# Kernel optimization log

Measured on AMD Instinct MI355X. Metric: run time of the kernel, lower is better.

## Reference

```python
import jax, jax.numpy as jnp
import numpy as np

NEG_INF = -1e9


def setup_inputs() -> dict:
    key = jax.random.key(0)
    k1, k2, k3 = jax.random.split(key, 3)
    B, S, D, N, K = 8, 4096, 1024, 128, 8
    hidden_states = jax.random.normal(k1, (B, S, D), dtype=jnp.float32)
    sentence_indicator = jnp.sort(
        jax.random.randint(k2, (B, S), 0, N), axis=-1).astype(jnp.int64)
    cls_w = jax.random.normal(k3, (D,), dtype=jnp.float32) * (1.0 / np.sqrt(D))
    cls_b = jnp.zeros((), dtype=jnp.float32)
    return {
        "hidden_states": hidden_states,
        "sentence_indicator": sentence_indicator,
        "cls_w": cls_w,
        "cls_b": cls_b,
        "num_sentences": N,
        "extraction_k": K,
    }


def _selection_loop(hidden_states, sentence_indicator, cls_w, cls_b,
                    num_sentences, extraction_k):
    # --- sentence segment-sum pooling (replaces per-sentence masked-sum loop) ---
    seg_sum = jax.vmap(
        lambda h, ind: jax.ops.segment_sum(h, ind, num_segments=num_sentences)
    )(hidden_states, sentence_indicator)               # [B, N, D]
    counts = jax.vmap(
        lambda ind: jax.ops.segment_sum(
            jnp.ones(ind.shape, jnp.float32), ind, num_segments=num_sentences)
    )(sentence_indicator)                              # [B, N]
    sentence_lens = jnp.clip(counts, 1.0)[..., None]   # [B, N, 1], clamp(min=1)
    sentence_mask0 = (counts > 0).astype(jnp.float32)  # valid-sentence mask [B, N]

    B, N, D = seg_sum.shape

    def step(carry, _):
        cur_sum, cur_len, smask, sel = carry
        combined = cur_sum[:, None, :] + seg_sum           # [B, N, D]
        combined_len = cur_len[:, None, :] + sentence_lens  # [B, N, 1]
        pooled = combined / combined_len                    # [B, N, D]
        logits = jnp.einsum('bnd,d->bn', pooled, cls_w) + cls_b
        logits = jnp.where(smask > 0, logits, NEG_INF)      # mask_tensor
        idx = jnp.argmax(logits, axis=-1)                   # eval path (argmax)
        one_hot = jax.nn.one_hot(idx, N, dtype=jnp.float32)  # [B, N]
        smask = (1.0 - one_hot) * smask
        new_sum = jnp.einsum('bn,bnd->bd', one_hot, combined)
        new_len = jnp.sum(one_hot[..., None] * combined_len, axis=1)  # [B, 1]
        return (new_sum, new_len, smask, sel + one_hot), logits

    init = (jnp.zeros((B, D), jnp.float32),
            jnp.zeros((B, 1), jnp.float32),
            sentence_mask0,
            jnp.zeros((B, N), jnp.float32))
    (_, _, _, selected), all_logits = jax.lax.scan(
        step, init, None, length=extraction_k)
    selected = jnp.clip(selected, 0.0, 1.0)  # clamp(max=1)
    return selected, all_logits  # [B,N], [K,B,N]


def reference(hidden_states, sentence_indicator, cls_w, cls_b,
              num_sentences, extraction_k):
    selected_one_hot, all_logits = _selection_loop(
        hidden_states, sentence_indicator, cls_w, cls_b,
        num_sentences, extraction_k)
    # convert_attention_mask: token is kept iff its sentence was selected
    new_attention_mask = jnp.take_along_axis(
        selected_one_hot, sentence_indicator, axis=1)      # [B, S] float 0/1
    masked_hidden_states = new_attention_mask[..., None] * hidden_states
    return selected_one_hot, all_logits, new_attention_mask, masked_hidden_states
```

## Files before the change

### kernel.cpp

```cpp
#include <hip/hip_runtime.h>

#define B_ 8
#define S_ 4096
#define D_ 1024
#define N_ 128
#define K_ 8
#define NEG_INF_ (-1e9f)

__global__ void tok_dot_kernel(const float* __restrict__ h,
                               const float* __restrict__ cls_w,
                               float* __restrict__ tok_dot) {
    const int lane = threadIdx.x & 63;
    const int gw = (blockIdx.x << 2) + (threadIdx.x >> 6);
    const int dofs = lane * 4;

    const float4 w0 = *reinterpret_cast<const float4*>(cls_w + 0 * 256 + dofs);
    const float4 w1 = *reinterpret_cast<const float4*>(cls_w + 1 * 256 + dofs);
    const float4 w2 = *reinterpret_cast<const float4*>(cls_w + 2 * 256 + dofs);
    const float4 w3 = *reinterpret_cast<const float4*>(cls_w + 3 * 256 + dofs);

    for (int token = gw; token < B_ * S_; token += 8192) {
        const float* p = h + (size_t)token * D_;
        const float4 v0 = *reinterpret_cast<const float4*>(p + 0 * 256 + dofs);
        const float4 v1 = *reinterpret_cast<const float4*>(p + 1 * 256 + dofs);
        const float4 v2 = *reinterpret_cast<const float4*>(p + 2 * 256 + dofs);
        const float4 v3 = *reinterpret_cast<const float4*>(p + 3 * 256 + dofs);
        float acc = v0.x * w0.x + v0.y * w0.y + v0.z * w0.z + v0.w * w0.w
                  + v1.x * w1.x + v1.y * w1.y + v1.z * w1.z + v1.w * w1.w
                  + v2.x * w2.x + v2.y * w2.y + v2.z * w2.z + v2.w * w2.w
                  + v3.x * w3.x + v3.y * w3.y + v3.z * w3.z + v3.w * w3.w;
        for (int off = 32; off > 0; off >>= 1) acc += __shfl_down(acc, off, 64);
        if (lane == 0) tok_dot[token] = acc;
    }
}

__global__ void select_kernel(const float* __restrict__ tok_dot,
                              const int* __restrict__ ind,
                              const float* __restrict__ cls_b,
                              float* __restrict__ out_selected,
                              float* __restrict__ out_logits,
                              float* __restrict__ sel_ws) {
    const int b = blockIdx.x;
    const int tid = threadIdx.x;

    __shared__ float td[S_];
    __shared__ int   si[S_];
    __shared__ float red_val[N_];
    __shared__ int   red_idx[N_];
    __shared__ float s_dotcur, s_lencur;

    for (int s = tid; s < S_; s += 256) {
        td[s] = tok_dot[b * S_ + s];
        si[s] = ind[b * S_ + s];
    }
    if (tid == 0) { s_dotcur = 0.f; s_lencur = 0.f; }
    __syncthreads();

    float dseg = 0.f, len = 1.f, smask = 0.f, sel = 0.f;
    if (tid < N_) {
        const int n = tid;
        int lo = 0, hi = S_;
        while (lo < hi) { int mid = (lo + hi) >> 1; if (si[mid] < n) lo = mid + 1; else hi = mid; }
        const int s0 = lo;
        lo = s0; hi = S_;
        while (lo < hi) { int mid = (lo + hi) >> 1; if (si[mid] < n + 1) lo = mid + 1; else hi = mid; }
        const int s1 = lo;
        float acc = 0.f;
        for (int s = s0; s < s1; ++s) acc += td[s];
        dseg  = acc;
        len   = fmaxf((float)(s1 - s0), 1.0f);
        smask = (s1 > s0) ? 1.f : 0.f;
    }
    const float bias = cls_b[0];
    __syncthreads();

    for (int k = 0; k < K_; ++k) {
        if (tid < N_) {
            float logit = (s_dotcur + dseg) / (s_lencur + len) + bias;
            logit = (smask > 0.f) ? logit : NEG_INF_;
            out_logits[(size_t)k * (B_ * N_) + b * N_ + tid] = logit;
            red_val[tid] = logit;
            red_idx[tid] = tid;
        }
        __syncthreads();
        for (int off = 64; off > 0; off >>= 1) {
            if (tid < off) {
                float v2 = red_val[tid + off]; int i2 = red_idx[tid + off];
                if (v2 > red_val[tid] || (v2 == red_val[tid] && i2 < red_idx[tid])) {
                    red_val[tid] = v2; red_idx[tid] = i2;
                }
            }
            __syncthreads();
        }
        const int pick = red_idx[0];
        if (tid == pick) {
            smask = 0.f; sel = 1.f;
            s_dotcur += dseg;
            s_lencur += len;
        }
        __syncthreads();
    }

    if (tid < N_) {
        out_selected[b * N_ + tid] = sel;
        sel_ws[b * N_ + tid] = sel;
    }
}

__global__ void mask_kernel(const float* __restrict__ h,
                            const int* __restrict__ ind,
                            const float* __restrict__ sel_ws,
                            float* __restrict__ out_mask,
                            float* __restrict__ out_masked) {
    const int t0 = blockIdx.x << 2;
    const int tid = threadIdx.x;
    #pragma unroll
    for (int i = 0; i < 4; ++i) {
        const int token = t0 + i;
        const int b = token >> 12;
        const float m = sel_ws[b * N_ + ind[token]];
        if (tid == 0) out_mask[token] = m;
        const size_t base = (size_t)token * D_ + tid * 4;
        if (m == 0.f) {
            *reinterpret_cast<float4*>(out_masked + base) = make_float4(0.f, 0.f, 0.f, 0.f);
        } else {
            const float4 v = *reinterpret_cast<const float4*>(h + base);
            *reinterpret_cast<float4*>(out_masked + base) =
                make_float4(v.x * m, v.y * m, v.z * m, v.w * m);
        }
    }
}

extern "C" void kernel_launch(void* const* d_in, const int* in_sizes, int n_in,
                              void* d_out, int out_size, void* d_ws, size_t ws_size,
                              hipStream_t stream) {
    const float* h     = (const float*)d_in[0];
    const int*   ind   = (const int*)d_in[1];
    const float* cls_w = (const float*)d_in[2];
    const float* cls_b = (const float*)d_in[3];

    float* out = (float*)d_out;
    float* out_selected = out;
    float* out_logits   = out + 1024;
    float* out_mask     = out + 1024 + 8192;
    float* out_masked   = out + 1024 + 8192 + 32768;

    char* ws = (char*)d_ws;
    float* tok_dot = (float*)ws;
    float* sel_ws  = (float*)(ws + (size_t)B_ * S_ * 4);

    tok_dot_kernel<<<dim3(2048), dim3(256), 0, stream>>>(h, cls_w, tok_dot);
    select_kernel<<<dim3(B_), dim3(256), 0, stream>>>(tok_dot, ind, cls_b,
                                                      out_selected, out_logits, sel_ws);
    mask_kernel<<<dim3(B_ * S_ / 4), dim3(256), 0, stream>>>(h, ind, sel_ws, out_mask, out_masked);
}
```

Baseline: 58.44 us.

## Zero-fill masked output separately and copy only selected sentence rows

The per-token mask kernel is replaced by three steps: a bulk zero-fill of the masked output, the selection kernel now also writing the token mask and the token ranges of the picked sentences, and a sparse copy kernel that copies only the selected tokens' hidden rows. Since only K of N sentences are selected, most rows need no read of the hidden states. This avoids the per-token indicator lookup and the full hidden-state read for unselected tokens. The cost is an extra full-size write pass plus another launch, and every sparse-copy block recomputes prefix counts from the ranges.

```diff
diff --git a/kernel.cpp b/kernel.cpp
--- a/kernel.cpp
+++ b/kernel.cpp
@@ -6,6 +6,13 @@
 #define N_ 128
 #define K_ 8
 #define NEG_INF_ (-1e9f)
+
+__global__ void zero_fill_kernel(float4* __restrict__ p, int n4) {
+    int i = blockIdx.x * blockDim.x + threadIdx.x;
+    const int stride = gridDim.x * blockDim.x;
+    const float4 z = make_float4(0.f, 0.f, 0.f, 0.f);
+    for (; i < n4; i += stride) p[i] = z;
+}
 
 __global__ void tok_dot_kernel(const float* __restrict__ h,
                                const float* __restrict__ cls_w,
@@ -39,7 +46,8 @@
                               const float* __restrict__ cls_b,
                               float* __restrict__ out_selected,
                               float* __restrict__ out_logits,
-                              float* __restrict__ sel_ws) {
+                              float* __restrict__ out_mask,
+                              int* __restrict__ ranges) {
     const int b = blockIdx.x;
     const int tid = threadIdx.x;
 
@@ -48,6 +56,9 @@
     __shared__ float red_val[N_];
     __shared__ int   red_idx[N_];
     __shared__ float s_dotcur, s_lencur;
+    __shared__ int   s_picks[K_];
+    __shared__ int   seg0[N_], seg1[N_];
+    __shared__ float sel_sh[N_];
 
     for (int s = tid; s < S_; s += 256) {
         td[s] = tok_dot[b * S_ + s];
@@ -65,6 +76,7 @@
         lo = s0; hi = S_;
         while (lo < hi) { int mid = (lo + hi) >> 1; if (si[mid] < n + 1) lo = mid + 1; else hi = mid; }
         const int s1 = lo;
+        seg0[tid] = s0; seg1[tid] = s1;
         float acc = 0.f;
         for (int s = s0; s < s1; ++s) acc += td[s];
         dseg  = acc;
@@ -97,37 +109,58 @@
             smask = 0.f; sel = 1.f;
             s_dotcur += dseg;
             s_lencur += len;
+            s_picks[k] = pick;
         }
         __syncthreads();
     }
 
     if (tid < N_) {
+        sel_sh[tid] = sel;
         out_selected[b * N_ + tid] = sel;
-        sel_ws[b * N_ + tid] = sel;
+    }
+    __syncthreads();
+    if (tid < K_) {
+        const int p = s_picks[tid];
+        ranges[(b * K_ + tid) * 2]     = seg0[p];
+        ranges[(b * K_ + tid) * 2 + 1] = seg1[p];
+    }
+    for (int s = tid; s < S_; s += 256) {
+        out_mask[b * S_ + s] = sel_sh[si[s]];
     }
 }
 
-__global__ void mask_kernel(const float* __restrict__ h,
-                            const int* __restrict__ ind,
-                            const float* __restrict__ sel_ws,
-                            float* __restrict__ out_mask,
-                            float* __restrict__ out_masked) {
-    const int t0 = blockIdx.x << 2;
+__global__ void sparse_copy_kernel(const float* __restrict__ h,
+                                   const int* __restrict__ ranges,
+                                   float* __restrict__ out_masked) {
+    int bpref[B_ + 1];
+    bpref[0] = 0;
+    #pragma unroll
+    for (int b = 0; b < B_; ++b) {
+        int c = 0;
+        #pragma unroll
+        for (int k = 0; k < K_; ++k)
+            c += ranges[(b * K_ + k) * 2 + 1] - ranges[(b * K_ + k) * 2];
+        bpref[b + 1] = bpref[b] + c;
+    }
+    const int total = bpref[B_];
     const int tid = threadIdx.x;
-    #pragma unroll
-    for (int i = 0; i < 4; ++i) {
-        const int token = t0 + i;
-        const int b = token >> 12;
-        const float m = sel_ws[b * N_ + ind[token]];
-        if (tid == 0) out_mask[token] = m;
-        const size_t base = (size_t)token * D_ + tid * 4;
-        if (m == 0.f) {
-            *reinterpret_cast<float4*>(out_masked + base) = make_float4(0.f, 0.f, 0.f, 0.f);
-        } else {
-            const float4 v = *reinterpret_cast<const float4*>(h + base);
-            *reinterpret_cast<float4*>(out_masked + base) =
-                make_float4(v.x * m, v.y * m, v.z * m, v.w * m);
+
+    for (int w = blockIdx.x; w < total; w += gridDim.x) {
+        int b = 0;
+        while (w >= bpref[b + 1]) ++b;
+        int off = w - bpref[b];
+        int s = 0;
+        #pragma unroll
+        for (int k = 0; k < K_; ++k) {
+            const int s0 = ranges[(b * K_ + k) * 2];
+            const int s1 = ranges[(b * K_ + k) * 2 + 1];
+            const int l = s1 - s0;
+            if (off < l) { s = s0 + off; off = 0x7fffffff; }
+            else if (off != 0x7fffffff) off -= l;
         }
+        const size_t base = ((size_t)b * S_ + s) * D_ + tid * 4;
+        *reinterpret_cast<float4*>(out_masked + base) =
+            *reinterpret_cast<const float4*>(h + base);
     }
 }
 
@@ -147,10 +180,14 @@
 
     char* ws = (char*)d_ws;
     float* tok_dot = (float*)ws;
-    float* sel_ws  = (float*)(ws + (size_t)B_ * S_ * 4);
+    int*   ranges  = (int*)(ws + (size_t)B_ * S_ * 4);
 
+    const int n4 = B_ * S_ * D_ / 4;
+    zero_fill_kernel<<<dim3(2048), dim3(256), 0, stream>>>(
+        reinterpret_cast<float4*>(out_masked), n4);
     tok_dot_kernel<<<dim3(2048), dim3(256), 0, stream>>>(h, cls_w, tok_dot);
     select_kernel<<<dim3(B_), dim3(256), 0, stream>>>(tok_dot, ind, cls_b,
-                                                      out_selected, out_logits, sel_ws);
-    mask_kernel<<<dim3(B_ * S_ / 4), dim3(256), 0, stream>>>(h, ind, sel_ws, out_mask, out_masked);
+                                                      out_selected, out_logits,
+                                                      out_mask, ranges);
+    sparse_copy_kernel<<<dim3(2048), dim3(256), 0, stream>>>(h, ranges, out_masked);
 }
```

After: 63.89 us. +9.3%, slower.

## Warp-level argmax in selection, move mask gather into select kernel, batch tokens

Applied to the files above, without the earlier changes.

The selection loop now runs in a single 64-lane wavefront, with each lane owning two sentences and doing the argmax through shuffles, so the shared-memory tree reduction and its many block barriers are gone. The select kernel also writes the per-token attention mask directly, which lets the final write kernel read one precomputed mask value per token instead of gathering indicator and selection per token. It also processes 8 tokens per block and copies h without multiplying, which is valid because the mask is 0 or 1. The tok_dot kernel unrolls two independent tokens per iteration to raise memory-level parallelism. The cost is extra serial work in the 8-block select kernel, which now also writes the mask.

```diff
diff --git a/kernel.cpp b/kernel.cpp
--- a/kernel.cpp
+++ b/kernel.cpp
@@ -19,18 +19,33 @@
     const float4 w2 = *reinterpret_cast<const float4*>(cls_w + 2 * 256 + dofs);
     const float4 w3 = *reinterpret_cast<const float4*>(cls_w + 3 * 256 + dofs);
 
-    for (int token = gw; token < B_ * S_; token += 8192) {
-        const float* p = h + (size_t)token * D_;
-        const float4 v0 = *reinterpret_cast<const float4*>(p + 0 * 256 + dofs);
-        const float4 v1 = *reinterpret_cast<const float4*>(p + 1 * 256 + dofs);
-        const float4 v2 = *reinterpret_cast<const float4*>(p + 2 * 256 + dofs);
-        const float4 v3 = *reinterpret_cast<const float4*>(p + 3 * 256 + dofs);
-        float acc = v0.x * w0.x + v0.y * w0.y + v0.z * w0.z + v0.w * w0.w
-                  + v1.x * w1.x + v1.y * w1.y + v1.z * w1.z + v1.w * w1.w
-                  + v2.x * w2.x + v2.y * w2.y + v2.z * w2.z + v2.w * w2.w
-                  + v3.x * w3.x + v3.y * w3.y + v3.z * w3.z + v3.w * w3.w;
-        for (int off = 32; off > 0; off >>= 1) acc += __shfl_down(acc, off, 64);
-        if (lane == 0) tok_dot[token] = acc;
+    #pragma unroll
+    for (int t = 0; t < 2; ++t) {
+        const int tokA = gw + t * 16384;
+        const int tokB = tokA + 8192;
+        const float* pA = h + (size_t)tokA * D_;
+        const float* pB = h + (size_t)tokB * D_;
+        const float4 a0 = *reinterpret_cast<const float4*>(pA + 0 * 256 + dofs);
+        const float4 a1 = *reinterpret_cast<const float4*>(pA + 1 * 256 + dofs);
+        const float4 a2 = *reinterpret_cast<const float4*>(pA + 2 * 256 + dofs);
+        const float4 a3 = *reinterpret_cast<const float4*>(pA + 3 * 256 + dofs);
+        const float4 b0 = *reinterpret_cast<const float4*>(pB + 0 * 256 + dofs);
+        const float4 b1 = *reinterpret_cast<const float4*>(pB + 1 * 256 + dofs);
+        const float4 b2 = *reinterpret_cast<const float4*>(pB + 2 * 256 + dofs);
+        const float4 b3 = *reinterpret_cast<const float4*>(pB + 3 * 256 + dofs);
+        float accA = a0.x * w0.x + a0.y * w0.y + a0.z * w0.z + a0.w * w0.w
+                   + a1.x * w1.x + a1.y * w1.y + a1.z * w1.z + a1.w * w1.w
+                   + a2.x * w2.x + a2.y * w2.y + a2.z * w2.z + a2.w * w2.w
+                   + a3.x * w3.x + a3.y * w3.y + a3.z * w3.z + a3.w * w3.w;
+        float accB = b0.x * w0.x + b0.y * w0.y + b0.z * w0.z + b0.w * w0.w
+                   + b1.x * w1.x + b1.y * w1.y + b1.z * w1.z + b1.w * w1.w
+                   + b2.x * w2.x + b2.y * w2.y + b2.z * w2.z + b2.w * w2.w
+                   + b3.x * w3.x + b3.y * w3.y + b3.z * w3.z + b3.w * w3.w;
+        for (int off = 32; off > 0; off >>= 1) {
+            accA += __shfl_down(accA, off, 64);
+            accB += __shfl_down(accB, off, 64);
+        }
+        if (lane == 0) { tok_dot[tokA] = accA; tok_dot[tokB] = accB; }
     }
 }
 
@@ -39,24 +54,20 @@
                               const float* __restrict__ cls_b,
                               float* __restrict__ out_selected,
                               float* __restrict__ out_logits,
-                              float* __restrict__ sel_ws) {
+                              float* __restrict__ out_mask) {
     const int b = blockIdx.x;
     const int tid = threadIdx.x;
 
     __shared__ float td[S_];
     __shared__ int   si[S_];
-    __shared__ float red_val[N_];
-    __shared__ int   red_idx[N_];
-    __shared__ float s_dotcur, s_lencur;
+    __shared__ float sh_dseg[N_], sh_len[N_], sh_msk[N_], sh_sel[N_];
 
     for (int s = tid; s < S_; s += 256) {
         td[s] = tok_dot[b * S_ + s];
         si[s] = ind[b * S_ + s];
     }
-    if (tid == 0) { s_dotcur = 0.f; s_lencur = 0.f; }
     __syncthreads();
 
-    float dseg = 0.f, len = 1.f, smask = 0.f, sel = 0.f;
     if (tid < N_) {
         const int n = tid;
         int lo = 0, hi = S_;
@@ -67,66 +78,70 @@
         const int s1 = lo;
         float acc = 0.f;
         for (int s = s0; s < s1; ++s) acc += td[s];
-        dseg  = acc;
-        len   = fmaxf((float)(s1 - s0), 1.0f);
-        smask = (s1 > s0) ? 1.f : 0.f;
+        sh_dseg[tid] = acc;
+        sh_len[tid]  = fmaxf((float)(s1 - s0), 1.0f);
+        sh_msk[tid]  = (s1 > s0) ? 1.f : 0.f;
     }
-    const float bias = cls_b[0];
     __syncthreads();
 
-    for (int k = 0; k < K_; ++k) {
-        if (tid < N_) {
-            float logit = (s_dotcur + dseg) / (s_lencur + len) + bias;
-            logit = (smask > 0.f) ? logit : NEG_INF_;
-            out_logits[(size_t)k * (B_ * N_) + b * N_ + tid] = logit;
-            red_val[tid] = logit;
-            red_idx[tid] = tid;
+    if (tid < 64) {
+        const float bias = cls_b[0];
+        const float d0 = sh_dseg[tid],      d1 = sh_dseg[tid + 64];
+        const float l0 = sh_len[tid],       l1 = sh_len[tid + 64];
+        float m0 = sh_msk[tid],             m1 = sh_msk[tid + 64];
+        float sel0 = 0.f, sel1 = 0.f;
+        float dot = 0.f, len = 0.f;
+
+        for (int k = 0; k < K_; ++k) {
+            const float lg0 = (m0 > 0.f) ? (dot + d0) / (len + l0) + bias : NEG_INF_;
+            const float lg1 = (m1 > 0.f) ? (dot + d1) / (len + l1) + bias : NEG_INF_;
+            out_logits[(size_t)k * (B_ * N_) + b * N_ + tid]      = lg0;
+            out_logits[(size_t)k * (B_ * N_) + b * N_ + tid + 64] = lg1;
+            float bv; int bi;
+            if (lg0 >= lg1) { bv = lg0; bi = tid; } else { bv = lg1; bi = tid + 64; }
+            for (int off = 32; off > 0; off >>= 1) {
+                const float ov = __shfl_xor(bv, off, 64);
+                const int   oi = __shfl_xor(bi, off, 64);
+                if (ov > bv || (ov == bv && oi < bi)) { bv = ov; bi = oi; }
+            }
+            const float dsrc = (bi < 64) ? d0 : d1;
+            const float lsrc = (bi < 64) ? l0 : l1;
+            dot += __shfl(dsrc, bi & 63, 64);
+            len += __shfl(lsrc, bi & 63, 64);
+            if ((bi & 63) == tid) {
+                if (bi < 64) { m0 = 0.f; sel0 = 1.f; }
+                else         { m1 = 0.f; sel1 = 1.f; }
+            }
         }
-        __syncthreads();
-        for (int off = 64; off > 0; off >>= 1) {
-            if (tid < off) {
-                float v2 = red_val[tid + off]; int i2 = red_idx[tid + off];
-                if (v2 > red_val[tid] || (v2 == red_val[tid] && i2 < red_idx[tid])) {
-                    red_val[tid] = v2; red_idx[tid] = i2;
-                }
-            }
-            __syncthreads();
-        }
-        const int pick = red_idx[0];
-        if (tid == pick) {
-            smask = 0.f; sel = 1.f;
-            s_dotcur += dseg;
-            s_lencur += len;
-        }
-        __syncthreads();
+        out_selected[b * N_ + tid]      = sel0;
+        out_selected[b * N_ + tid + 64] = sel1;
+        sh_sel[tid]      = sel0;
+        sh_sel[tid + 64] = sel1;
     }
-
-    if (tid < N_) {
-        out_selected[b * N_ + tid] = sel;
-        sel_ws[b * N_ + tid] = sel;
+    __syncthreads();
+    for (int s = tid; s < S_; s += 256) {
+        out_mask[b * S_ + s] = sh_sel[si[s]];
     }
 }
 
-__global__ void mask_kernel(const float* __restrict__ h,
-                            const int* __restrict__ ind,
-                            const float* __restrict__ sel_ws,
-                            float* __restrict__ out_mask,
-                            float* __restrict__ out_masked) {
-    const int t0 = blockIdx.x << 2;
+#define TPB_ 8
+__global__ void write_kernel(const float* __restrict__ h,
+                             const float* __restrict__ out_mask,
+                             float* __restrict__ out_masked) {
+    const int t0 = blockIdx.x * TPB_;
     const int tid = threadIdx.x;
+    float m[TPB_];
     #pragma unroll
-    for (int i = 0; i < 4; ++i) {
-        const int token = t0 + i;
-        const int b = token >> 12;
-        const float m = sel_ws[b * N_ + ind[token]];
-        if (tid == 0) out_mask[token] = m;
-        const size_t base = (size_t)token * D_ + tid * 4;
-        if (m == 0.f) {
-            *reinterpret_cast<float4*>(out_masked + base) = make_float4(0.f, 0.f, 0.f, 0.f);
+    for (int i = 0; i < TPB_; ++i) m[i] = out_mask[t0 + i];
+    const float4 z = make_float4(0.f, 0.f, 0.f, 0.f);
+    #pragma unroll
+    for (int i = 0; i < TPB_; ++i) {
+        const size_t base = (size_t)(t0 + i) * D_ + tid * 4;
+        if (m[i] == 0.f) {
+            *reinterpret_cast<float4*>(out_masked + base) = z;
         } else {
-            const float4 v = *reinterpret_cast<const float4*>(h + base);
             *reinterpret_cast<float4*>(out_masked + base) =
-                make_float4(v.x * m, v.y * m, v.z * m, v.w * m);
+                *reinterpret_cast<const float4*>(h + base);
         }
     }
 }
@@ -145,12 +160,11 @@
     float* out_mask     = out + 1024 + 8192;
     float* out_masked   = out + 1024 + 8192 + 32768;
 
-    char* ws = (char*)d_ws;
-    float* tok_dot = (float*)ws;
-    float* sel_ws  = (float*)(ws + (size_t)B_ * S_ * 4);
+    float* tok_dot = (float*)d_ws;
 
     tok_dot_kernel<<<dim3(2048), dim3(256), 0, stream>>>(h, cls_w, tok_dot);
     select_kernel<<<dim3(B_), dim3(256), 0, stream>>>(tok_dot, ind, cls_b,
-                                                      out_selected, out_logits, sel_ws);
-    mask_kernel<<<dim3(B_ * S_ / 4), dim3(256), 0, stream>>>(h, ind, sel_ws, out_mask, out_masked);
+                                                      out_selected, out_logits,
+                                                      out_mask);
+    write_kernel<<<dim3(B_ * S_ / TPB_), dim3(256), 0, stream>>>(h, out_mask, out_masked);
 }
```

Result: faster. 56.68 us (-3.0%).
